# Kernel optimization log

Hardware: AMD Instinct MI355X
Metric: run time of the kernel (lower is better)

Reference implementation:

```python
import jax, jax.numpy as jnp
import numpy as np

N_NODES = 100000
N_EDGES = 1600000
D_IN, D_HID, N_CLS = 256, 128, 47


def setup_inputs() -> dict:
    key = jax.random.key(0)
    k = jax.random.split(key, 5)
    x = jax.random.normal(k[0], (N_NODES, D_IN), dtype=jnp.float32)
    edge_index = jax.random.randint(k[1], (2, N_EDGES), 0, N_NODES, dtype=jnp.int64)
    W1 = jax.random.normal(k[2], (D_IN, D_HID), dtype=jnp.float32) * 0.05
    b1 = jnp.zeros((D_HID,), dtype=jnp.float32)
    W2 = jax.random.normal(k[3], (D_HID, N_CLS), dtype=jnp.float32) * 0.05
    b2 = jnp.zeros((N_CLS,), dtype=jnp.float32)
    return {"x": x, "edge_index": edge_index, "W1": W1, "b1": b1, "W2": W2, "b2": b2}


def _gcn_conv(x, W, b, src, dst, norm, n):
    # PyG GCNConv: linear transform, normalized scatter-add aggregation, bias after
    h = x @ W                                   # [N, D_out]
    msg = h[src] * norm[:, None]                # gather over edges [E', D_out]
    agg = jax.ops.segment_sum(msg, dst, num_segments=n)
    return agg + b


def reference(x, edge_index, W1, b1, W2, b2):
    n = x.shape[0]
    loop = jnp.arange(n, dtype=edge_index.dtype)
    src = jnp.concatenate([edge_index[0], loop])  # add self-loops
    dst = jnp.concatenate([edge_index[1], loop])
    # symmetric normalization D^-1/2 (A+I) D^-1/2 (degree = in-degree incl. self-loop)
    deg = jax.ops.segment_sum(jnp.ones_like(dst, dtype=x.dtype), dst, num_segments=n)
    dinv = jnp.where(deg > 0, jax.lax.rsqrt(deg), 0.0)
    norm = dinv[src] * dinv[dst]                 # [E']
    h1 = jax.nn.relu(_gcn_conv(x, W1, b1, src, dst, norm, n))
    # dropout with training=False is identity
    out = _gcn_conv(h1, W2, b2, src, dst, norm, n)
    return out
```

## Files before the change

kernel.cpp:

```cpp
#include <hip/hip_runtime.h>
#include <hip/hip_bf16.h>

#define DIN 256
#define DHID 128
#define NCLS 47
#define BSHIFT 9
#define BNODES 512
#define NPART 256
#define BCAPS 9216
#define CHUNKE 6400

typedef __attribute__((ext_vector_type(8))) short short8;
typedef __attribute__((ext_vector_type(4))) float f32x4;

__device__ __forceinline__ short f2bf(float f) {
    __bf16 b = (__bf16)f;
    return __builtin_bit_cast(short, b);
}
__device__ __forceinline__ float bfu(unsigned int u) {
    return __uint_as_float(u << 16);
}
__device__ __forceinline__ float bfh(unsigned int u) {
    return __uint_as_float(u & 0xffff0000u);
}
__device__ __forceinline__ unsigned int pack2(float lo, float hi) {
    return (unsigned int)(unsigned short)f2bf(lo)
         | ((unsigned int)(unsigned short)f2bf(hi) << 16);
}
__device__ __forceinline__ void add8(float* a, uint4 v) {
    a[0] += bfu(v.x); a[1] += bfh(v.x);
    a[2] += bfu(v.y); a[3] += bfh(v.y);
    a[4] += bfu(v.z); a[5] += bfh(v.z);
    a[6] += bfu(v.w); a[7] += bfh(v.w);
}
__device__ __forceinline__ void fma8(float* a, uint4 v, float d) {
    a[0] += d * bfu(v.x); a[1] += d * bfh(v.x);
    a[2] += d * bfu(v.y); a[3] += d * bfh(v.y);
    a[4] += d * bfu(v.z); a[5] += d * bfh(v.z);
    a[6] += d * bfu(v.w); a[7] += d * bfh(v.w);
}

__global__ __launch_bounds__(256) void k_prep_hist(const float* __restrict__ W1,
                                                   const float* __restrict__ W2,
                                                   short* __restrict__ W1s,
                                                   short* __restrict__ W2s,
                                                   const int* __restrict__ dst,
                                                   int* __restrict__ ghist,
                                                   int E, int NB, int chunk) {
    __shared__ int lh[256];
    int blk = blockIdx.x, t = threadIdx.x;
    if (blk < 16) {
        int tid = blk * 256 + t;
        int frag = tid >> 6, lane = tid & 63;
        int kt = frag >> 3, nt = frag & 7;
        int quad = lane >> 4, col = lane & 15;
        #pragma unroll
        for (int j = 0; j < 8; ++j) {
            int k = kt * 32 + quad * 8 + j;
            W1s[(size_t)tid * 8 + j] = f2bf(W1[k * DHID + nt * 16 + col]);
        }
    } else if (blk < 20) {
        int tid = (blk - 16) * 256 + t;
        int frag = tid >> 6, lane = tid & 63;
        int kt = frag >> 2, nt = frag & 3;
        int quad = lane >> 4, col = lane & 15;
        int c = nt * 16 + col;
        #pragma unroll
        for (int j = 0; j < 8; ++j) {
            int k = kt * 32 + quad * 8 + j;
            float v = (c < NCLS) ? W2[k * NCLS + c] : 0.0f;
            W2s[(size_t)tid * 8 + j] = f2bf(v);
        }
    } else {
        int p = blk - 20;
        for (int i = t; i < NB; i += 256) lh[i] = 0;
        __syncthreads();
        int lo = p * chunk, hi = min(E, lo + chunk);
        for (int i = lo + t; i < hi; i += 256)
            atomicAdd(&lh[dst[i] >> BSHIFT], 1);
        __syncthreads();
        for (int i = t; i < NB; i += 256) ghist[(size_t)i * NPART + p] = lh[i];
    }
}

__global__ __launch_bounds__(256) void k_scatter_gemm1(const int* __restrict__ src,
                                                       const int* __restrict__ dst,
                                                       const int* __restrict__ ghist,
                                                       int* __restrict__ btot,
                                                       unsigned int* __restrict__ bbuf,
                                                       int E, int NB, int chunk,
                                                       const float* __restrict__ x,
                                                       const short* __restrict__ W1s,
                                                       short* __restrict__ hb, int n) {
    __shared__ __align__(16) char smem[65536];
    int blk = blockIdx.x, t = threadIdx.x;

    if (blk < NPART) {
        unsigned int* stage = (unsigned int*)smem;
        int* sdest = (int*)(smem + 25600);
        int* lcur  = (int*)(smem + 51200);
        int* gdst  = (int*)(smem + 52224);
        int* wsum  = (int*)(smem + 53248);

        int tot = 0, pref = 0, mine = 0;
        if (t < NB) {
            const int* gp = ghist + (size_t)t * NPART;
            mine = gp[blk];
            #pragma unroll 8
            for (int p = 0; p < NPART; ++p) {
                int v = gp[p];
                tot += v;
                pref += (p < blk) ? v : 0;
            }
        }
        if (blk == 0 && t < NB) btot[t] = tot;

        int lane = t & 63, w = t >> 6;
        int incl = tot;
        #pragma unroll
        for (int off = 1; off < 64; off <<= 1) {
            int u = __shfl_up(incl, off, 64);
            if (lane >= off) incl += u;
        }
        if (lane == 63) wsum[w] = incl;
        __syncthreads();
        int wadd = 0;
        for (int i = 0; i < w; ++i) wadd += wsum[i];
        int bbase = wadd + incl - tot;
        __syncthreads();
        incl = mine;
        #pragma unroll
        for (int off = 1; off < 64; off <<= 1) {
            int u = __shfl_up(incl, off, 64);
            if (lane >= off) incl += u;
        }
        if (lane == 63) wsum[w] = incl;
        __syncthreads();
        wadd = 0;
        for (int i = 0; i < w; ++i) wadd += wsum[i];
        int ex = wadd + incl - mine;

        lcur[t] = ex;
        gdst[t] = bbase + pref - ex;
        __syncthreads();

        int lo = blk * chunk, hi = min(E, lo + chunk), cnt = hi - lo;
        for (int i = lo + t; i < hi; i += 256) {
            int d = dst[i];
            int b = d >> BSHIFT;
            int slot = atomicAdd(&lcur[b], 1);
            stage[slot] = (unsigned int)src[i] | ((unsigned int)(d & (BNODES - 1)) << 17);
            sdest[slot] = gdst[b] + slot;
        }
        __syncthreads();
        for (int i = t; i < cnt; i += 256)
            bbuf[sdest[i]] = stage[i];
    } else {
        short* lw = (short*)smem;
        {
            const uint4* g = (const uint4*)W1s;
            uint4* l = (uint4*)lw;
            for (int i = t; i < 4096; i += 256) l[i] = g[i];
        }
        __syncthreads();

        int bid = blk - NPART;
        int wave = t >> 6, lane = t & 63;
        int quad = lane >> 4, lrow = lane & 15;
        long long rowbase = (long long)bid * 128 + wave * 32;

        f32x4 acc[2][8];
        #pragma unroll
        for (int rt = 0; rt < 2; ++rt)
            #pragma unroll
            for (int nt = 0; nt < 8; ++nt) acc[rt][nt] = (f32x4){0.f, 0.f, 0.f, 0.f};

        const short8* lf = (const short8*)lw;

        #pragma unroll
        for (int kt = 0; kt < 8; ++kt) {
            int k0 = kt * 32 + quad * 8;
            short8 a[2];
            #pragma unroll
            for (int rt = 0; rt < 2; ++rt) {
                long long row = rowbase + rt * 16 + lrow;
                float4 v0 = {0.f,0.f,0.f,0.f}, v1 = {0.f,0.f,0.f,0.f};
                if (row < n) {
                    const float* xp = x + row * DIN + k0;
                    v0 = *(const float4*)xp;
                    v1 = *(const float4*)(xp + 4);
                }
                short8 av;
                av[0] = f2bf(v0.x); av[1] = f2bf(v0.y); av[2] = f2bf(v0.z); av[3] = f2bf(v0.w);
                av[4] = f2bf(v1.x); av[5] = f2bf(v1.y); av[6] = f2bf(v1.z); av[7] = f2bf(v1.w);
                a[rt] = av;
            }
            #pragma unroll
            for (int nt = 0; nt < 8; ++nt) {
                short8 b = lf[(kt * 8 + nt) * 64 + lane];
                acc[0][nt] = __builtin_amdgcn_mfma_f32_16x16x32_bf16(a[0], b, acc[0][nt], 0, 0, 0);
                acc[1][nt] = __builtin_amdgcn_mfma_f32_16x16x32_bf16(a[1], b, acc[1][nt], 0, 0, 0);
            }
        }
        #pragma unroll
        for (int rt = 0; rt < 2; ++rt)
            #pragma unroll
            for (int nt = 0; nt < 8; ++nt)
                #pragma unroll
                for (int r = 0; r < 4; ++r) {
                    long long row = rowbase + rt * 16 + quad * 4 + r;
                    if (row < n) hb[row * DHID + nt * 16 + lrow] = f2bf(acc[rt][nt][r]);
                }
    }
}

__device__ __forceinline__ void scan_btot(const int* __restrict__ btot, int NB,
                                          int* lbase, int* wsum) {
    int t = threadIdx.x;
    int v = (t < NB) ? btot[t] : 0;
    int incl = v;
    int lane = t & 63, w = t >> 6;
    #pragma unroll
    for (int off = 1; off < 64; off <<= 1) {
        int u = __shfl_up(incl, off, 64);
        if (lane >= off) incl += u;
    }
    if (lane == 63) wsum[w] = incl;
    __syncthreads();
    int wadd = 0;
    for (int i = 0; i < w; ++i) wadd += wsum[i];
    lbase[t] = wadd + incl - v;
    __syncthreads();
}

__global__ __launch_bounds__(256) void k_bsort(const int* __restrict__ btot,
                                               unsigned int* __restrict__ bbuf,
                                               int* __restrict__ degi,
                                               int* __restrict__ beg,
                                               float* __restrict__ dinv, int n, int NB) {
    __shared__ unsigned int stage[BCAPS];
    __shared__ int hist[BNODES];
    __shared__ int cur[BNODES];
    __shared__ int lbase[256];
    __shared__ int wsum[4];

    int b = blockIdx.x, t = threadIdx.x;
    scan_btot(btot, NB, lbase, wsum);
    int cnt = min(btot[b], BCAPS);
    int gbase = lbase[b];
    int node0 = b << BSHIFT;

    if (t < 128) { ((int2*)hist)[t] = (int2){0, 0}; ((int2*)hist)[t + 128] = (int2){0, 0}; }
    __syncthreads();

    for (int i = t; i < cnt; i += 256) {
        unsigned int p = bbuf[gbase + i];
        stage[i] = p;
        atomicAdd(&hist[p >> 17], 1);
    }
    __syncthreads();

    int v0 = hist[2 * t], v1 = hist[2 * t + 1];
    int s = v0 + v1;
    int incl = s;
    int lane = t & 63, w = t >> 6;
    #pragma unroll
    for (int off = 1; off < 64; off <<= 1) {
        int u = __shfl_up(incl, off, 64);
        if (lane >= off) incl += u;
    }
    if (lane == 63) wsum[w] = incl;
    __syncthreads();
    int wadd = 0;
    for (int i = 0; i < w; ++i) wadd += wsum[i];
    int ex = wadd + incl - s;
    cur[2 * t] = ex;
    cur[2 * t + 1] = ex + v0;
    int nodeA = node0 + 2 * t, nodeB = node0 + 2 * t + 1;
    if (nodeA < n) {
        degi[nodeA] = v0;
        beg[nodeA]  = gbase + ex;
        dinv[nodeA] = rsqrtf((float)(v0 + 1));
    }
    if (nodeB < n) {
        degi[nodeB] = v1;
        beg[nodeB]  = gbase + ex + v0;
        dinv[nodeB] = rsqrtf((float)(v1 + 1));
    }
    __syncthreads();

    for (int i = t; i < cnt; i += 256) {
        unsigned int p = stage[i];
        int slot = atomicAdd(&cur[p >> 17], 1);
        bbuf[gbase + slot] = p & 0x1FFFFu;
    }
}

__global__ __launch_bounds__(256) void k_gather1(const int* __restrict__ beg,
                          const int* __restrict__ degi,
                          const int* __restrict__ ssrc, const float* __restrict__ dinv,
                          const uint4* __restrict__ hb4, const float* __restrict__ b1,
                          uint4* __restrict__ h1u4, int n) {
    int node = blockIdx.x * 4 + (threadIdx.x >> 6);
    int t = threadIdx.x & 63;
    if (node >= n) return;
    int cnt = degi[node];
    int bg  = beg[node];
    int grp = t >> 4, sub = t & 15;

    float a[8] = {0.f,0.f,0.f,0.f,0.f,0.f,0.f,0.f};
    int k = 0;
    for (; k + 16 <= cnt; k += 16) {
        int s[4];
        #pragma unroll
        for (int q = 0; q < 4; ++q) s[q] = ssrc[bg + k + grp * 4 + q];
        float dv[4]; uint4 v[4];
        #pragma unroll
        for (int q = 0; q < 4; ++q) { dv[q] = dinv[s[q]]; v[q] = hb4[(size_t)s[q] * 16 + sub]; }
        #pragma unroll
        for (int q = 0; q < 4; ++q) fma8(a, v[q], dv[q]);
    }
    for (; k < cnt; k += 4) {
        int idx = k + grp;
        if (idx < cnt) {
            int s = ssrc[bg + idx];
            fma8(a, hb4[(size_t)s * 16 + sub], dinv[s]);
        }
    }

    #pragma unroll
    for (int j = 0; j < 8; ++j) {
        a[j] += __shfl_xor(a[j], 16);
        a[j] += __shfl_xor(a[j], 32);
    }

    if (grp == 0) {
        uint4 sv = hb4[(size_t)node * 16 + sub];
        float di = dinv[node], dd = di * di;
        float4 bA = ((const float4*)b1)[sub * 2];
        float4 bB = ((const float4*)b1)[sub * 2 + 1];
        float v0 = fmaxf(di * a[0] + dd * bfu(sv.x) + bA.x, 0.f);
        float v1 = fmaxf(di * a[1] + dd * bfh(sv.x) + bA.y, 0.f);
        float v2 = fmaxf(di * a[2] + dd * bfu(sv.y) + bA.z, 0.f);
        float v3 = fmaxf(di * a[3] + dd * bfh(sv.y) + bA.w, 0.f);
        float v4 = fmaxf(di * a[4] + dd * bfu(sv.z) + bB.x, 0.f);
        float v5 = fmaxf(di * a[5] + dd * bfh(sv.z) + bB.y, 0.f);
        float v6 = fmaxf(di * a[6] + dd * bfu(sv.w) + bB.z, 0.f);
        float v7 = fmaxf(di * a[7] + dd * bfh(sv.w) + bB.w, 0.f);
        uint4 o;
        o.x = pack2(v0, v1);
        o.y = pack2(v2, v3);
        o.z = pack2(v4, v5);
        o.w = pack2(v6, v7);
        h1u4[(size_t)node * 16 + sub] = o;
    }
}

__global__ __launch_bounds__(256) void k_gemm2_mfma(const short* __restrict__ h1b,
                                                    const short* __restrict__ W2s,
                                                    const float* __restrict__ dinv,
                                                    short* __restrict__ h2b, int n) {
    __shared__ short lw[8192];
    {
        const uint4* g = (const uint4*)W2s;
        uint4* l = (uint4*)lw;
        for (int i = threadIdx.x; i < 1024; i += 256) l[i] = g[i];
    }
    __syncthreads();

    int wave = threadIdx.x >> 6, lane = threadIdx.x & 63;
    int quad = lane >> 4, lrow = lane & 15;
    long long row0 = (long long)blockIdx.x * 64 + wave * 16;

    f32x4 acc[4];
    #pragma unroll
    for (int nt = 0; nt < 4; ++nt) acc[nt] = (f32x4){0.f, 0.f, 0.f, 0.f};

    const short8* lf = (const short8*)lw;

    #pragma unroll
    for (int kt = 0; kt < 4; ++kt) {
        long long row = row0 + lrow;
        short8 a = (short8){0,0,0,0,0,0,0,0};
        if (row < n) a = *(const short8*)(h1b + row * DHID + kt * 32 + quad * 8);
        #pragma unroll
        for (int nt = 0; nt < 4; ++nt)
            acc[nt] = __builtin_amdgcn_mfma_f32_16x16x32_bf16(a, lf[(kt * 4 + nt) * 64 + lane], acc[nt], 0, 0, 0);
    }
    float dvv[4];
    #pragma unroll
    for (int r = 0; r < 4; ++r) {
        long long row = row0 + quad * 4 + r;
        dvv[r] = (row < n) ? dinv[row] : 0.f;
    }
    #pragma unroll
    for (int nt = 0; nt < 4; ++nt)
        #pragma unroll
        for (int r = 0; r < 4; ++r) {
            long long row = row0 + quad * 4 + r;
            if (row < n) h2b[row * 64 + nt * 16 + lrow] = f2bf(acc[nt][r] * dvv[r]);
        }
}

__global__ __launch_bounds__(256) void k_gather2(const int* __restrict__ beg,
                          const int* __restrict__ degi,
                          const int* __restrict__ ssrc, const float* __restrict__ dinv,
                          const uint4* __restrict__ h2b4, const float* __restrict__ b2,
                          float* __restrict__ out, int n) {
    int node = blockIdx.x * 4 + (threadIdx.x >> 6);
    int t = threadIdx.x & 63;
    if (node >= n) return;
    int cnt = degi[node];
    int bg  = beg[node];
    int grp = t >> 3, sub = t & 7;

    float a[8] = {0.f,0.f,0.f,0.f,0.f,0.f,0.f,0.f};
    int k = 0;
    for (; k + 16 <= cnt; k += 16) {
        int s0 = ssrc[bg + k + grp], s1 = ssrc[bg + k + 8 + grp];
        uint4 v0 = h2b4[(size_t)s0 * 8 + sub];
        uint4 v1 = h2b4[(size_t)s1 * 8 + sub];
        add8(a, v0); add8(a, v1);
    }
    for (; k < cnt; k += 8) {
        int idx = k + grp;
        if (idx < cnt) {
            int s = ssrc[bg + idx];
            add8(a, h2b4[(size_t)s * 8 + sub]);
        }
    }
    if (grp == 0) add8(a, h2b4[(size_t)node * 8 + sub]);

    #pragma unroll
    for (int j = 0; j < 8; ++j) {
        a[j] += __shfl_xor(a[j], 8);
        a[j] += __shfl_xor(a[j], 16);
        a[j] += __shfl_xor(a[j], 32);
    }

    if (grp == 0) {
        float di = dinv[node];
        #pragma unroll
        for (int j = 0; j < 8; ++j) {
            int c = sub * 8 + j;
            if (c < NCLS) out[(size_t)node * NCLS + c] = di * a[j] + b2[c];
        }
    }
}

extern "C" void kernel_launch(void* const* d_in, const int* in_sizes, int n_in,
                              void* d_out, int out_size, void* d_ws, size_t ws_size,
                              hipStream_t stream) {
    const float* x  = (const float*)d_in[0];
    const int*   ei = (const int*)d_in[1];
    const float* W1 = (const float*)d_in[2];
    const float* b1 = (const float*)d_in[3];
    const float* W2 = (const float*)d_in[4];
    const float* b2 = (const float*)d_in[5];

    const int n = in_sizes[0] / DIN;
    const int E = in_sizes[1] / 2;
    const int* src = ei;
    const int* dst = ei + E;
    float* out = (float*)d_out;

    const int NB = (n + BNODES - 1) >> BSHIFT;
    const int chunk = (E + NPART - 1) / NPART;

    char* w = (char*)d_ws;
    int*   ghist = (int*)w;                    w += (size_t)NB * NPART * 4;
    int*   btot  = (int*)w;                    w += ((size_t)NB * 4 + 15) & ~15ull;
    int*   degi  = (int*)w;                    w += (size_t)n * 4;
    int*   beg   = (int*)w;                    w += (size_t)n * 4;
    float* dinv  = (float*)w;                  w += (size_t)n * 4;
    short* W1s   = (short*)w;                  w += (size_t)32768 * 2;
    short* W2s   = (short*)w;                  w += (size_t)8192 * 2;
    unsigned int* bbuf = (unsigned int*)w;     w += (size_t)E * 4;
    short* hb    = (short*)w;                  w += (size_t)n * DHID * 2;
    short* h1b   = (short*)w;                  w += (size_t)n * DHID * 2;
    short* h2b   = (short*)w;                  w += (size_t)n * 64 * 2;

    k_prep_hist<<<20 + NPART, 256, 0, stream>>>(W1, W2, W1s, W2s, dst, ghist, E, NB, chunk);
    k_scatter_gemm1<<<NPART + (n + 127) / 128, 256, 0, stream>>>(src, dst, ghist, btot, bbuf,
                                                                 E, NB, chunk, x, W1s, hb, n);
    k_bsort<<<NB, 256, 0, stream>>>(btot, bbuf, degi, beg, dinv, n, NB);
    k_gather1<<<(n + 3) / 4, 256, 0, stream>>>(beg, degi, (const int*)bbuf, dinv,
                                               (const uint4*)hb, b1,
                                               (uint4*)h1b, n);
    k_gemm2_mfma<<<(n + 63) / 64, 256, 0, stream>>>(h1b, W2s, dinv, h2b, n);
    k_gather2<<<(n + 3) / 4, 256, 0, stream>>>(beg, degi, (const int*)bbuf, dinv,
                                               (const uint4*)h2b, b2, out, n);
}
```

Baseline: 402.6 us.

## Split edge partitioning finer, add column-scan kernel, shrink layer-2 feature width

Raises the edge partition count from 256 to 1024 so the scatter work is split into more, smaller chunks. A new k_colscan kernel precomputes per-bucket partition offsets, replacing the redundant per-block loop over all partitions in the scatter kernel. The GEMM1 path now reads W1 fragments directly from global memory instead of staging them in LDS. k_bsort moves to 512 threads, and the layer-2 hidden buffer shrinks from 64 to 48 bf16 columns per row, which cuts gather2 traffic but leaves two of eight lanes per group idle. The cost is an extra kernel launch, larger histogram buffers, and possibly worse reuse of W1 in GEMM1.

Result: faster. 367.8 us (-8.7%).

```diff
diff --git a/kernel.cpp b/kernel.cpp
--- a/kernel.cpp
+++ b/kernel.cpp
@@ -6,9 +6,9 @@
 #define NCLS 47
 #define BSHIFT 9
 #define BNODES 512
-#define NPART 256
+#define NPART 1024
 #define BCAPS 9216
-#define CHUNKE 6400
+#define CHUNKE 1600
 
 typedef __attribute__((ext_vector_type(8))) short short8;
 typedef __attribute__((ext_vector_type(4))) float f32x4;
@@ -83,40 +83,75 @@
     }
 }
 
+__global__ __launch_bounds__(256) void k_colscan(const int* __restrict__ ghist,
+                                                 int* __restrict__ goff,
+                                                 int* __restrict__ btot) {
+    __shared__ int wsum[4];
+    int b = blockIdx.x, t = threadIdx.x;
+    int4 v = ((const int4*)(ghist + (size_t)b * NPART))[t];
+    int s = v.x + v.y + v.z + v.w;
+    int incl = s;
+    int lane = t & 63, w = t >> 6;
+    #pragma unroll
+    for (int off = 1; off < 64; off <<= 1) {
+        int u = __shfl_up(incl, off, 64);
+        if (lane >= off) incl += u;
+    }
+    if (lane == 63) wsum[w] = incl;
+    __syncthreads();
+    int wadd = 0;
+    for (int i = 0; i < w; ++i) wadd += wsum[i];
+    int ex = wadd + incl - s;
+    int4 o;
+    o.x = ex; o.y = ex + v.x; o.z = o.y + v.y; o.w = o.z + v.z;
+    ((int4*)(goff + (size_t)b * NPART))[t] = o;
+    if (t == 255) btot[b] = wadd + incl;
+}
+
+__device__ __forceinline__ void scan_btot(const int* __restrict__ btot, int NB,
+                                          int* lbase, int* wsum) {
+    int t = threadIdx.x;
+    int v = (t < NB) ? btot[t] : 0;
+    int incl = v;
+    int lane = t & 63, w = t >> 6;
+    #pragma unroll
+    for (int off = 1; off < 64; off <<= 1) {
+        int u = __shfl_up(incl, off, 64);
+        if (lane >= off) incl += u;
+    }
+    if (lane == 63) wsum[w] = incl;
+    __syncthreads();
+    int wadd = 0;
+    for (int i = 0; i < w; ++i) wadd += wsum[i];
+    lbase[t] = wadd + incl - v;
+    __syncthreads();
+}
+
 __global__ __launch_bounds__(256) void k_scatter_gemm1(const int* __restrict__ src,
                                                        const int* __restrict__ dst,
                                                        const int* __restrict__ ghist,
-                                                       int* __restrict__ btot,
+                                                       const int* __restrict__ goff,
+                                                       const int* __restrict__ btot,
                                                        unsigned int* __restrict__ bbuf,
                                                        int E, int NB, int chunk,
                                                        const float* __restrict__ x,
                                                        const short* __restrict__ W1s,
                                                        short* __restrict__ hb, int n) {
-    __shared__ __align__(16) char smem[65536];
+    __shared__ unsigned int stage[CHUNKE];
+    __shared__ int sdest[CHUNKE];
+    __shared__ int lcur[256];
+    __shared__ int gdst[256];
+    __shared__ int wsum[4];
+
     int blk = blockIdx.x, t = threadIdx.x;
 
     if (blk < NPART) {
-        unsigned int* stage = (unsigned int*)smem;
-        int* sdest = (int*)(smem + 25600);
-        int* lcur  = (int*)(smem + 51200);
-        int* gdst  = (int*)(smem + 52224);
-        int* wsum  = (int*)(smem + 53248);
-
-        int tot = 0, pref = 0, mine = 0;
-        if (t < NB) {
-            const int* gp = ghist + (size_t)t * NPART;
-            mine = gp[blk];
-            #pragma unroll 8
-            for (int p = 0; p < NPART; ++p) {
-                int v = gp[p];
-                tot += v;
-                pref += (p < blk) ? v : 0;
-            }
-        }
-        if (blk == 0 && t < NB) btot[t] = tot;
-
+        int p = blk;
+        scan_btot(btot, NB, gdst, wsum);
+
+        int mine = (t < NB) ? ghist[(size_t)t * NPART + p] : 0;
+        int incl = mine;
         int lane = t & 63, w = t >> 6;
-        int incl = tot;
         #pragma unroll
         for (int off = 1; off < 64; off <<= 1) {
             int u = __shfl_up(incl, off, 64);
@@ -126,25 +161,12 @@
         __syncthreads();
         int wadd = 0;
         for (int i = 0; i < w; ++i) wadd += wsum[i];
-        int bbase = wadd + incl - tot;
+        int ex = wadd + incl - mine;
+        lcur[t] = ex;
+        if (t < NB) gdst[t] += goff[(size_t)t * NPART + p] - ex;
         __syncthreads();
-        incl = mine;
-        #pragma unroll
-        for (int off = 1; off < 64; off <<= 1) {
-            int u = __shfl_up(incl, off, 64);
-            if (lane >= off) incl += u;
-        }
-        if (lane == 63) wsum[w] = incl;
-        __syncthreads();
-        wadd = 0;
-        for (int i = 0; i < w; ++i) wadd += wsum[i];
-        int ex = wadd + incl - mine;
-
-        lcur[t] = ex;
-        gdst[t] = bbase + pref - ex;
-        __syncthreads();
-
-        int lo = blk * chunk, hi = min(E, lo + chunk), cnt = hi - lo;
+
+        int lo = p * chunk, hi = min(E, lo + chunk), cnt = hi - lo;
         for (int i = lo + t; i < hi; i += 256) {
             int d = dst[i];
             int b = d >> BSHIFT;
@@ -156,14 +178,6 @@
         for (int i = t; i < cnt; i += 256)
             bbuf[sdest[i]] = stage[i];
     } else {
-        short* lw = (short*)smem;
-        {
-            const uint4* g = (const uint4*)W1s;
-            uint4* l = (uint4*)lw;
-            for (int i = t; i < 4096; i += 256) l[i] = g[i];
-        }
-        __syncthreads();
-
         int bid = blk - NPART;
         int wave = t >> 6, lane = t & 63;
         int quad = lane >> 4, lrow = lane & 15;
@@ -175,7 +189,7 @@
             #pragma unroll
             for (int nt = 0; nt < 8; ++nt) acc[rt][nt] = (f32x4){0.f, 0.f, 0.f, 0.f};
 
-        const short8* lf = (const short8*)lw;
+        const short8* lf = (const short8*)W1s;
 
         #pragma unroll
         for (int kt = 0; kt < 8; ++kt) {
@@ -214,26 +228,7 @@
     }
 }
 
-__device__ __forceinline__ void scan_btot(const int* __restrict__ btot, int NB,
-                                          int* lbase, int* wsum) {
-    int t = threadIdx.x;
-    int v = (t < NB) ? btot[t] : 0;
-    int incl = v;
-    int lane = t & 63, w = t >> 6;
-    #pragma unroll
-    for (int off = 1; off < 64; off <<= 1) {
-        int u = __shfl_up(incl, off, 64);
-        if (lane >= off) incl += u;
-    }
-    if (lane == 63) wsum[w] = incl;
-    __syncthreads();
-    int wadd = 0;
-    for (int i = 0; i < w; ++i) wadd += wsum[i];
-    lbase[t] = wadd + incl - v;
-    __syncthreads();
-}
-
-__global__ __launch_bounds__(256) void k_bsort(const int* __restrict__ btot,
+__global__ __launch_bounds__(512) void k_bsort(const int* __restrict__ btot,
                                                unsigned int* __restrict__ bbuf,
                                                int* __restrict__ degi,
                                                int* __restrict__ beg,
@@ -245,51 +240,85 @@
     __shared__ int wsum[4];
 
     int b = blockIdx.x, t = threadIdx.x;
-    scan_btot(btot, NB, lbase, wsum);
+
+    if (t < 256) {
+        int v = (t < NB) ? btot[t] : 0;
+        int incl = v;
+        int lane = t & 63, w = t >> 6;
+        #pragma unroll
+        for (int off = 1; off < 64; off <<= 1) {
+            int u = __shfl_up(incl, off, 64);
+            if (lane >= off) incl += u;
+        }
+        if (lane == 63) wsum[w] = incl;
+        lbase[t] = v;
+    }
+    __syncthreads();
+    if (t < 256) {
+        int v = lbase[t];
+        int incl = v;
+        int lane = t & 63, w = t >> 6;
+        #pragma unroll
+        for (int off = 1; off < 64; off <<= 1) {
+            int u = __shfl_up(incl, off, 64);
+            if (lane >= off) incl += u;
+        }
+        int wadd = 0;
+        for (int i = 0; i < w; ++i) wadd += wsum[i];
+        lbase[t] = wadd + incl - v;
+    }
+    hist[t] = 0;
+    __syncthreads();
+
     int cnt = min(btot[b], BCAPS);
     int gbase = lbase[b];
     int node0 = b << BSHIFT;
 
-    if (t < 128) { ((int2*)hist)[t] = (int2){0, 0}; ((int2*)hist)[t + 128] = (int2){0, 0}; }
-    __syncthreads();
-
-    for (int i = t; i < cnt; i += 256) {
+    for (int i = t; i < cnt; i += 512) {
         unsigned int p = bbuf[gbase + i];
         stage[i] = p;
         atomicAdd(&hist[p >> 17], 1);
     }
     __syncthreads();
 
-    int v0 = hist[2 * t], v1 = hist[2 * t + 1];
-    int s = v0 + v1;
-    int incl = s;
-    int lane = t & 63, w = t >> 6;
-    #pragma unroll
-    for (int off = 1; off < 64; off <<= 1) {
-        int u = __shfl_up(incl, off, 64);
-        if (lane >= off) incl += u;
-    }
-    if (lane == 63) wsum[w] = incl;
-    __syncthreads();
-    int wadd = 0;
-    for (int i = 0; i < w; ++i) wadd += wsum[i];
-    int ex = wadd + incl - s;
-    cur[2 * t] = ex;
-    cur[2 * t + 1] = ex + v0;
-    int nodeA = node0 + 2 * t, nodeB = node0 + 2 * t + 1;
-    if (nodeA < n) {
-        degi[nodeA] = v0;
-        beg[nodeA]  = gbase + ex;
-        dinv[nodeA] = rsqrtf((float)(v0 + 1));
-    }
-    if (nodeB < n) {
-        degi[nodeB] = v1;
-        beg[nodeB]  = gbase + ex + v0;
-        dinv[nodeB] = rsqrtf((float)(v1 + 1));
-    }
-    __syncthreads();
-
-    for (int i = t; i < cnt; i += 256) {
+    int v0 = 0, v1 = 0, ex = 0;
+    if (t < 256) {
+        v0 = hist[2 * t]; v1 = hist[2 * t + 1];
+        int s = v0 + v1;
+        int incl = s;
+        int lane = t & 63, w = t >> 6;
+        #pragma unroll
+        for (int off = 1; off < 64; off <<= 1) {
+            int u = __shfl_up(incl, off, 64);
+            if (lane >= off) incl += u;
+        }
+        if (lane == 63) wsum[w] = incl;
+        ex = incl - s;
+    }
+    __syncthreads();
+    if (t < 256) {
+        int lane = t & 63, w = t >> 6;
+        (void)lane;
+        int wadd = 0;
+        for (int i = 0; i < w; ++i) wadd += wsum[i];
+        ex += wadd;
+        cur[2 * t] = ex;
+        cur[2 * t + 1] = ex + v0;
+        int nodeA = node0 + 2 * t, nodeB = node0 + 2 * t + 1;
+        if (nodeA < n) {
+            degi[nodeA] = v0;
+            beg[nodeA]  = gbase + ex;
+            dinv[nodeA] = rsqrtf((float)(v0 + 1));
+        }
+        if (nodeB < n) {
+            degi[nodeB] = v1;
+            beg[nodeB]  = gbase + ex + v0;
+            dinv[nodeB] = rsqrtf((float)(v1 + 1));
+        }
+    }
+    __syncthreads();
+
+    for (int i = t; i < cnt; i += 512) {
         unsigned int p = stage[i];
         int slot = atomicAdd(&cur[p >> 17], 1);
         bbuf[gbase + slot] = p & 0x1FFFFu;
@@ -372,9 +401,9 @@
     int quad = lane >> 4, lrow = lane & 15;
     long long row0 = (long long)blockIdx.x * 64 + wave * 16;
 
-    f32x4 acc[4];
-    #pragma unroll
-    for (int nt = 0; nt < 4; ++nt) acc[nt] = (f32x4){0.f, 0.f, 0.f, 0.f};
+    f32x4 acc[3];
+    #pragma unroll
+    for (int nt = 0; nt < 3; ++nt) acc[nt] = (f32x4){0.f, 0.f, 0.f, 0.f};
 
     const short8* lf = (const short8*)lw;
 
@@ -384,7 +413,7 @@
         short8 a = (short8){0,0,0,0,0,0,0,0};
         if (row < n) a = *(const short8*)(h1b + row * DHID + kt * 32 + quad * 8);
         #pragma unroll
-        for (int nt = 0; nt < 4; ++nt)
+        for (int nt = 0; nt < 3; ++nt)
             acc[nt] = __builtin_amdgcn_mfma_f32_16x16x32_bf16(a, lf[(kt * 4 + nt) * 64 + lane], acc[nt], 0, 0, 0);
     }
     float dvv[4];
@@ -394,18 +423,18 @@
         dvv[r] = (row < n) ? dinv[row] : 0.f;
     }
     #pragma unroll
-    for (int nt = 0; nt < 4; ++nt)
+    for (int nt = 0; nt < 3; ++nt)
         #pragma unroll
         for (int r = 0; r < 4; ++r) {
             long long row = row0 + quad * 4 + r;
-            if (row < n) h2b[row * 64 + nt * 16 + lrow] = f2bf(acc[nt][r] * dvv[r]);
+            if (row < n) h2b[row * 48 + nt * 16 + lrow] = f2bf(acc[nt][r] * dvv[r]);
         }
 }
 
 __global__ __launch_bounds__(256) void k_gather2(const int* __restrict__ beg,
                           const int* __restrict__ degi,
                           const int* __restrict__ ssrc, const float* __restrict__ dinv,
-                          const uint4* __restrict__ h2b4, const float* __restrict__ b2,
+                          const uint4* __restrict__ h2b6, const float* __restrict__ b2,
                           float* __restrict__ out, int n) {
     int node = blockIdx.x * 4 + (threadIdx.x >> 6);
     int t = threadIdx.x & 63;
@@ -418,18 +447,20 @@
     int k = 0;
     for (; k + 16 <= cnt; k += 16) {
         int s0 = ssrc[bg + k + grp], s1 = ssrc[bg + k + 8 + grp];
-        uint4 v0 = h2b4[(size_t)s0 * 8 + sub];
-        uint4 v1 = h2b4[(size_t)s1 * 8 + sub];
-        add8(a, v0); add8(a, v1);
+        if (sub < 6) {
+            uint4 v0 = h2b6[(size_t)s0 * 6 + sub];
+            uint4 v1 = h2b6[(size_t)s1 * 6 + sub];
+            add8(a, v0); add8(a, v1);
+        }
     }
     for (; k < cnt; k += 8) {
         int idx = k + grp;
         if (idx < cnt) {
             int s = ssrc[bg + idx];
-            add8(a, h2b4[(size_t)s * 8 + sub]);
-        }
-    }
-    if (grp == 0) add8(a, h2b4[(size_t)node * 8 + sub]);
+            if (sub < 6) add8(a, h2b6[(size_t)s * 6 + sub]);
+        }
+    }
+    if (grp == 0 && sub < 6) add8(a, h2b6[(size_t)node * 6 + sub]);
 
     #pragma unroll
     for (int j = 0; j < 8; ++j) {
@@ -469,7 +500,8 @@
 
     char* w = (char*)d_ws;
     int*   ghist = (int*)w;                    w += (size_t)NB * NPART * 4;
-    int*   btot  = (int*)w;                    w += ((size_t)NB * 4 + 15) & ~15ull;
+    int*   goff  = (int*)w;                    w += (size_t)NB * NPART * 4;
+    int*   btot  = (int*)w;                    w += ((size_t)256 * 4);
     int*   degi  = (int*)w;                    w += (size_t)n * 4;
     int*   beg   = (int*)w;                    w += (size_t)n * 4;
     float* dinv  = (float*)w;                  w += (size_t)n * 4;
@@ -478,12 +510,14 @@
     unsigned int* bbuf = (unsigned int*)w;     w += (size_t)E * 4;
     short* hb    = (short*)w;                  w += (size_t)n * DHID * 2;
     short* h1b   = (short*)w;                  w += (size_t)n * DHID * 2;
-    short* h2b   = (short*)w;                  w += (size_t)n * 64 * 2;
+    short* h2b   = (short*)w;                  w += (size_t)n * 48 * 2;
 
     k_prep_hist<<<20 + NPART, 256, 0, stream>>>(W1, W2, W1s, W2s, dst, ghist, E, NB, chunk);
-    k_scatter_gemm1<<<NPART + (n + 127) / 128, 256, 0, stream>>>(src, dst, ghist, btot, bbuf,
-                                                                 E, NB, chunk, x, W1s, hb, n);
-    k_bsort<<<NB, 256, 0, stream>>>(btot, bbuf, degi, beg, dinv, n, NB);
+    k_colscan<<<NB, 256, 0, stream>>>(ghist, goff, btot);
+    k_scatter_gemm1<<<NPART + (n + 127) / 128, 256, 0, stream>>>(src, dst, ghist, goff, btot,
+                                                                 bbuf, E, NB, chunk,
+                                                                 x, W1s, hb, n);
+    k_bsort<<<NB, 512, 0, stream>>>(btot, bbuf, degi, beg, dinv, n, NB);
     k_gather1<<<(n + 3) / 4, 256, 0, stream>>>(beg, degi, (const int*)bbuf, dinv,
                                                (const uint4*)hb, b1,
                                                (uint4*)h1b, n);
```
